# Performance work log

Hardware: AMD Instinct MI355X
Metric: run time of the kernel (lower is better)

The kernel has to match this reference:

```python
import jax, jax.numpy as jnp
import numpy as np

ALPHA = 0.5
B = 4096
K = 8192


def setup_inputs() -> dict:
    key = jax.random.key(0)
    k1, k2 = jax.random.split(key)
    outputs = jax.random.normal(k1, (B, K), dtype=jnp.float32)
    labels = jax.random.randint(k2, (B,), 0, K)
    targets = jax.nn.one_hot(labels, K, dtype=jnp.float32)
    S = jnp.eye(K, dtype=jnp.float32)          # soft-label matrix (state)
    S_t = jnp.zeros((K, K), dtype=jnp.float32)  # running stats (state)
    count = jnp.zeros((K, 1), dtype=jnp.float32)
    return {"outputs": outputs, "targets": targets, "S": S, "S_t": S_t, "count": count}


def reference(outputs, targets, S, S_t, count):
    # loss path
    ls = jax.nn.log_softmax(outputs, axis=1)          # [B, K]
    bsz = outputs.shape[0]
    target_label = jnp.argmax(targets, axis=1)        # [B]
    prediction = jnp.argmax(outputs, axis=1)          # [B]
    soft_targets = S[target_label]                    # [B, K] gather
    ce_hard = -(ls * targets).sum() / bsz
    ce_soft = -(ls * soft_targets).sum() / bsz
    loss = ALPHA * ce_hard + (1.0 - ALPHA) * ce_soft

    # stats accumulation (the original python for-loop, as one fused scatter-add)
    probs = jax.nn.softmax(jax.lax.stop_gradient(outputs), axis=1)  # [B, K]
    correct = (prediction == target_label).astype(probs.dtype)      # [B]
    S_t_new = S_t + jax.ops.segment_sum(probs * correct[:, None], target_label, num_segments=K)
    count_new = count + jax.ops.segment_sum(correct, target_label, num_segments=K)[:, None]
    return loss, S_t_new, count_new
```

## Files before the change

### kernel.cpp

```cpp
#include <hip/hip_runtime.h>
#include <math.h>

#define K 8192
#define BROWS 4096
#define ALPHA 0.5f

__device__ __forceinline__ void argmax_combine(float& v, int& i, float v2, int i2){
  if (v2 > v || (v2 == v && i2 < i)) { v = v2; i = i2; }
}

__global__ __launch_bounds__(256) void row_stats_kernel(
    const float* __restrict__ outputs,
    const float* __restrict__ targets,
    const float* __restrict__ S,
    float* __restrict__ rowloss,
    int*   __restrict__ rowtl,
    int*   __restrict__ rowcorrect,
    float* __restrict__ rowm,
    float* __restrict__ rowinvZ)
{
  const int b = blockIdx.x;
  const int t = threadIdx.x;
  const int lane = t & 63;
  const int wid  = t >> 6;

  const float4* orow = (const float4*)(outputs + (size_t)b * K);
  float x[32];
#pragma unroll
  for (int i = 0; i < 8; ++i){
    float4 v = orow[i*256 + t];
    x[4*i+0]=v.x; x[4*i+1]=v.y; x[4*i+2]=v.z; x[4*i+3]=v.w;
  }

  float mv = -INFINITY; int mi = 0x7fffffff;
#pragma unroll
  for (int i = 0; i < 8; ++i){
#pragma unroll
    for (int c = 0; c < 4; ++c){
      int idx = i*1024 + t*4 + c;
      argmax_combine(mv, mi, x[4*i+c], idx);
    }
  }

  const float4* trow = (const float4*)(targets + (size_t)b * K);
  float tv = -INFINITY; int ti = 0x7fffffff;
  float d_hard = 0.f, s_hard = 0.f;
#pragma unroll
  for (int i = 0; i < 8; ++i){
    float4 v = trow[i*256 + t];
    float tc[4] = {v.x, v.y, v.z, v.w};
#pragma unroll
    for (int c = 0; c < 4; ++c){
      int idx = i*1024 + t*4 + c;
      d_hard += x[4*i+c] * tc[c];
      s_hard += tc[c];
      argmax_combine(tv, ti, tc[c], idx);
    }
  }

#pragma unroll
  for (int off = 32; off; off >>= 1){
    float v2 = __shfl_down(mv, off, 64); int i2 = __shfl_down(mi, off, 64);
    argmax_combine(mv, mi, v2, i2);
    v2 = __shfl_down(tv, off, 64); i2 = __shfl_down(ti, off, 64);
    argmax_combine(tv, ti, v2, i2);
  }

  __shared__ float s_v[2][4]; __shared__ int s_i[2][4];
  __shared__ float s_m; __shared__ int s_pred; __shared__ int s_tl;
  if (lane == 0){ s_v[0][wid]=mv; s_i[0][wid]=mi; s_v[1][wid]=tv; s_i[1][wid]=ti; }
  __syncthreads();
  if (t == 0){
    float av=s_v[0][0]; int ai=s_i[0][0];
    float bv=s_v[1][0]; int bi=s_i[1][0];
#pragma unroll
    for (int w=1; w<4; ++w){
      argmax_combine(av, ai, s_v[0][w], s_i[0][w]);
      argmax_combine(bv, bi, s_v[1][w], s_i[1][w]);
    }
    s_m = av; s_pred = ai; s_tl = bi;
  }
  __syncthreads();
  const float m  = s_m;
  const int   tl = s_tl;

  float se = 0.f;
#pragma unroll
  for (int i = 0; i < 32; ++i) se += expf(x[i] - m);

  const float4* srow = (const float4*)(S + (size_t)tl * K);
  float d_soft = 0.f, s_soft = 0.f;
#pragma unroll
  for (int i = 0; i < 8; ++i){
    float4 v = srow[i*256 + t];
    d_soft += x[4*i+0]*v.x + x[4*i+1]*v.y + x[4*i+2]*v.z + x[4*i+3]*v.w;
    s_soft += v.x + v.y + v.z + v.w;
  }

  float sums[5] = {d_hard, s_hard, se, d_soft, s_soft};
#pragma unroll
  for (int off = 32; off; off >>= 1){
#pragma unroll
    for (int j = 0; j < 5; ++j) sums[j] += __shfl_down(sums[j], off, 64);
  }
  __shared__ float s_sums[4][5];
  if (lane == 0){
#pragma unroll
    for (int j = 0; j < 5; ++j) s_sums[wid][j] = sums[j];
  }
  __syncthreads();
  if (t == 0){
    float tot[5];
#pragma unroll
    for (int j=0;j<5;++j) tot[j] = s_sums[0][j]+s_sums[1][j]+s_sums[2][j]+s_sums[3][j];
    float Z = tot[2];
    float logZ = logf(Z);
    float ceh = -(tot[0] - (m + logZ) * tot[1]);
    float ces = -(tot[3] - (m + logZ) * tot[4]);
    rowloss[b]    = (ALPHA * ceh + (1.0f - ALPHA) * ces) * (1.0f / (float)BROWS);
    rowtl[b]      = tl;
    rowcorrect[b] = (s_pred == tl) ? 1 : 0;
    rowm[b]       = m;
    rowinvZ[b]    = 1.0f / Z;
  }
}

__global__ __launch_bounds__(256) void copy_st_kernel(const float* __restrict__ src,
                                                      float* __restrict__ dst){
  size_t base = (size_t)blockIdx.x * 8192 + threadIdx.x;
#pragma unroll
  for (int j = 0; j < 32; ++j)
    dst[base + (size_t)j*256] = src[base + (size_t)j*256];
}

__global__ __launch_bounds__(256) void loss_count_kernel(const float* __restrict__ rowloss,
                                                         const float* __restrict__ count,
                                                         float* __restrict__ out_loss,
                                                         float* __restrict__ out_count){
  int t = threadIdx.x;
  float s = 0.f;
  for (int i = t; i < BROWS; i += 256) s += rowloss[i];
#pragma unroll
  for (int off = 32; off; off >>= 1) s += __shfl_down(s, off, 64);
  __shared__ float sh[4];
  if ((t & 63) == 0) sh[t >> 6] = s;
  __syncthreads();
  if (t == 0) out_loss[0] = sh[0] + sh[1] + sh[2] + sh[3];
  for (int i = t; i < K; i += 256) out_count[i] = count[i];
}

__global__ __launch_bounds__(256) void scatter_kernel(const float* __restrict__ outputs,
    const int* __restrict__ rowtl, const int* __restrict__ rowcorrect,
    const float* __restrict__ rowm, const float* __restrict__ rowinvZ,
    float* __restrict__ out_St, float* __restrict__ out_count){
  int b = blockIdx.x;
  if (!rowcorrect[b]) return;
  int tl = rowtl[b];
  float m = rowm[b], invZ = rowinvZ[b];
  const float* orow = outputs + (size_t)b * K;
  float* drow = out_St + (size_t)tl * K;
  for (int k = threadIdx.x; k < K; k += 256)
    atomicAdd(&drow[k], expf(orow[k] - m) * invZ);
  if (threadIdx.x == 0) atomicAdd(&out_count[tl], 1.0f);
}

extern "C" void kernel_launch(void* const* d_in, const int* in_sizes, int n_in,
                              void* d_out, int out_size, void* d_ws, size_t ws_size,
                              hipStream_t stream) {
  const float* outputs = (const float*)d_in[0];
  const float* targets = (const float*)d_in[1];
  const float* S       = (const float*)d_in[2];
  const float* S_t     = (const float*)d_in[3];
  const float* count   = (const float*)d_in[4];

  float* out       = (float*)d_out;
  float* out_loss  = out;
  float* out_St    = out + 1;
  float* out_count = out + 1 + (size_t)K * K;

  float* rowloss    = (float*)d_ws;
  float* rowm       = rowloss + BROWS;
  float* rowinvZ    = rowm + BROWS;
  int*   rowtl      = (int*)(rowinvZ + BROWS);
  int*   rowcorrect = rowtl + BROWS;

  hipLaunchKernelGGL(row_stats_kernel, dim3(BROWS), dim3(256), 0, stream,
                     outputs, targets, S, rowloss, rowtl, rowcorrect, rowm, rowinvZ);
  hipLaunchKernelGGL(copy_st_kernel, dim3(8192), dim3(256), 0, stream, S_t, out_St);
  hipLaunchKernelGGL(loss_count_kernel, dim3(1), dim3(256), 0, stream,
                     rowloss, count, out_loss, out_count);
  hipLaunchKernelGGL(scatter_kernel, dim3(BROWS), dim3(256), 0, stream,
                     outputs, rowtl, rowcorrect, rowm, rowinvZ, out_St, out_count);
}
```

Baseline: 727.6 us.

## Fuse row stats with S_t copy and merge loss reduction into scatter kernel

Interleaves row-statistics blocks with S_t copy blocks in a single launch so the compute-heavy row pass overlaps the bandwidth-bound 256MB copy. The copy writes aligned float4 stores to the output (offset by one float for the loss slot) while reading scalars, and the count copy rides along in one copy block. The loss reduction and count copy kernel is folded into an extra block of the scatter kernel, cutting the launch count from four to two. Reads of S_t become unaligned scalar loads, which could reduce read efficiency.

```diff
diff --git a/kernel.cpp b/kernel.cpp
--- a/kernel.cpp
+++ b/kernel.cpp
@@ -4,27 +4,71 @@
 #define K 8192
 #define BROWS 4096
 #define ALPHA 0.5f
+#define NTOT ((size_t)K * (size_t)K)
+#define VEC4 16777215
 
 __device__ __forceinline__ void argmax_combine(float& v, int& i, float v2, int i2){
   if (v2 > v || (v2 == v && i2 < i)) { v = v2; i = i2; }
 }
 
-__global__ __launch_bounds__(256) void row_stats_kernel(
+__global__ __launch_bounds__(256) void fused_kernel(
     const float* __restrict__ outputs,
     const float* __restrict__ targets,
     const float* __restrict__ S,
+    const float* __restrict__ S_t,
+    const float* __restrict__ count,
+    float* __restrict__ out,
     float* __restrict__ rowloss,
     int*   __restrict__ rowtl,
     int*   __restrict__ rowcorrect,
     float* __restrict__ rowm,
     float* __restrict__ rowinvZ)
 {
-  const int b = blockIdx.x;
-  const int t = threadIdx.x;
+  __shared__ float s_v[2][4]; __shared__ int s_i[2][4];
+  __shared__ float s_m; __shared__ int s_pred; __shared__ int s_tl;
+  __shared__ float s_sums[4][5];
+
+  const int bb = blockIdx.x;
+  const int r  = bb / 3;
+  const int m3 = bb - r * 3;
+  const int t  = threadIdx.x;
   const int lane = t & 63;
   const int wid  = t >> 6;
 
-  const float4* orow = (const float4*)(outputs + (size_t)b * K);
+  if (m3 != 0) {
+    const int cb = 2 * r + (m3 - 1);
+    float4* dst4 = (float4*)(out + 4);
+    const size_t base = (size_t)cb * 2048 + t;
+    if (cb != 8191) {
+#pragma unroll
+      for (int i = 0; i < 8; ++i) {
+        size_t d = base + (size_t)i * 256;
+        size_t e = 4 * d + 3;
+        float4 v; v.x = S_t[e]; v.y = S_t[e+1]; v.z = S_t[e+2]; v.w = S_t[e+3];
+        dst4[d] = v;
+      }
+    } else {
+#pragma unroll
+      for (int i = 0; i < 8; ++i) {
+        size_t d = base + (size_t)i * 256;
+        if (d < (size_t)VEC4) {
+          size_t e = 4 * d + 3;
+          float4 v; v.x = S_t[e]; v.y = S_t[e+1]; v.z = S_t[e+2]; v.w = S_t[e+3];
+          dst4[d] = v;
+        }
+      }
+    }
+    if (cb == 0) {
+      if (t < 3) out[1 + t] = S_t[t];
+      if (t == 3) out[NTOT] = S_t[NTOT - 1];
+    } else if (cb == 1) {
+      float* out_count = out + 1 + NTOT;
+      for (int i = t; i < K; i += 256) out_count[i] = count[i];
+    }
+    return;
+  }
+
+  const float4* orow = (const float4*)(outputs + (size_t)r * K);
   float x[32];
 #pragma unroll
   for (int i = 0; i < 8; ++i){
@@ -42,7 +86,7 @@
     }
   }
 
-  const float4* trow = (const float4*)(targets + (size_t)b * K);
+  const float4* trow = (const float4*)(targets + (size_t)r * K);
   float tv = -INFINITY; int ti = 0x7fffffff;
   float d_hard = 0.f, s_hard = 0.f;
 #pragma unroll
@@ -66,8 +110,6 @@
     argmax_combine(tv, ti, v2, i2);
   }
 
-  __shared__ float s_v[2][4]; __shared__ int s_i[2][4];
-  __shared__ float s_m; __shared__ int s_pred; __shared__ int s_tl;
   if (lane == 0){ s_v[0][wid]=mv; s_i[0][wid]=mi; s_v[1][wid]=tv; s_i[1][wid]=ti; }
   __syncthreads();
   if (t == 0){
@@ -103,7 +145,6 @@
 #pragma unroll
     for (int j = 0; j < 5; ++j) sums[j] += __shfl_down(sums[j], off, 64);
   }
-  __shared__ float s_sums[4][5];
   if (lane == 0){
 #pragma unroll
     for (int j = 0; j < 5; ++j) s_sums[wid][j] = sums[j];
@@ -117,51 +158,44 @@
     float logZ = logf(Z);
     float ceh = -(tot[0] - (m + logZ) * tot[1]);
     float ces = -(tot[3] - (m + logZ) * tot[4]);
-    rowloss[b]    = (ALPHA * ceh + (1.0f - ALPHA) * ces) * (1.0f / (float)BROWS);
-    rowtl[b]      = tl;
-    rowcorrect[b] = (s_pred == tl) ? 1 : 0;
-    rowm[b]       = m;
-    rowinvZ[b]    = 1.0f / Z;
-  }
-}
-
-__global__ __launch_bounds__(256) void copy_st_kernel(const float* __restrict__ src,
-                                                      float* __restrict__ dst){
-  size_t base = (size_t)blockIdx.x * 8192 + threadIdx.x;
-#pragma unroll
-  for (int j = 0; j < 32; ++j)
-    dst[base + (size_t)j*256] = src[base + (size_t)j*256];
-}
-
-__global__ __launch_bounds__(256) void loss_count_kernel(const float* __restrict__ rowloss,
-                                                         const float* __restrict__ count,
-                                                         float* __restrict__ out_loss,
-                                                         float* __restrict__ out_count){
-  int t = threadIdx.x;
-  float s = 0.f;
-  for (int i = t; i < BROWS; i += 256) s += rowloss[i];
-#pragma unroll
-  for (int off = 32; off; off >>= 1) s += __shfl_down(s, off, 64);
-  __shared__ float sh[4];
-  if ((t & 63) == 0) sh[t >> 6] = s;
-  __syncthreads();
-  if (t == 0) out_loss[0] = sh[0] + sh[1] + sh[2] + sh[3];
-  for (int i = t; i < K; i += 256) out_count[i] = count[i];
-}
-
-__global__ __launch_bounds__(256) void scatter_kernel(const float* __restrict__ outputs,
-    const int* __restrict__ rowtl, const int* __restrict__ rowcorrect,
-    const float* __restrict__ rowm, const float* __restrict__ rowinvZ,
-    float* __restrict__ out_St, float* __restrict__ out_count){
-  int b = blockIdx.x;
+    rowloss[r]    = (ALPHA * ceh + (1.0f - ALPHA) * ces) * (1.0f / (float)BROWS);
+    rowtl[r]      = tl;
+    rowcorrect[r] = (s_pred == tl) ? 1 : 0;
+    rowm[r]       = m;
+    rowinvZ[r]    = 1.0f / Z;
+  }
+}
+
+__global__ __launch_bounds__(256) void epilogue_kernel(
+    const float* __restrict__ outputs,
+    const float* __restrict__ rowloss,
+    const int*   __restrict__ rowtl,
+    const int*   __restrict__ rowcorrect,
+    const float* __restrict__ rowm,
+    const float* __restrict__ rowinvZ,
+    float* __restrict__ out)
+{
+  const int b = blockIdx.x;
+  const int t = threadIdx.x;
+  if (b == BROWS) {
+    float s = 0.f;
+    for (int i = t; i < BROWS; i += 256) s += rowloss[i];
+#pragma unroll
+    for (int off = 32; off; off >>= 1) s += __shfl_down(s, off, 64);
+    __shared__ float sh[4];
+    if ((t & 63) == 0) sh[t >> 6] = s;
+    __syncthreads();
+    if (t == 0) out[0] = sh[0] + sh[1] + sh[2] + sh[3];
+    return;
+  }
   if (!rowcorrect[b]) return;
-  int tl = rowtl[b];
-  float m = rowm[b], invZ = rowinvZ[b];
+  const int tl = rowtl[b];
+  const float m = rowm[b], invZ = rowinvZ[b];
   const float* orow = outputs + (size_t)b * K;
-  float* drow = out_St + (size_t)tl * K;
-  for (int k = threadIdx.x; k < K; k += 256)
+  float* drow = out + 1 + (size_t)tl * K;
+  for (int k = t; k < K; k += 256)
     atomicAdd(&drow[k], expf(orow[k] - m) * invZ);
-  if (threadIdx.x == 0) atomicAdd(&out_count[tl], 1.0f);
+  if (t == 0) atomicAdd(out + 1 + NTOT + tl, 1.0f);
 }
 
 extern "C" void kernel_launch(void* const* d_in, const int* in_sizes, int n_in,
@@ -173,10 +207,7 @@
   const float* S_t     = (const float*)d_in[3];
   const float* count   = (const float*)d_in[4];
 
-  float* out       = (float*)d_out;
-  float* out_loss  = out;
-  float* out_St    = out + 1;
-  float* out_count = out + 1 + (size_t)K * K;
+  float* out = (float*)d_out;
 
   float* rowloss    = (float*)d_ws;
   float* rowm       = rowloss + BROWS;
@@ -184,11 +215,9 @@
   int*   rowtl      = (int*)(rowinvZ + BROWS);
   int*   rowcorrect = rowtl + BROWS;
 
-  hipLaunchKernelGGL(row_stats_kernel, dim3(BROWS), dim3(256), 0, stream,
-                     outputs, targets, S, rowloss, rowtl, rowcorrect, rowm, rowinvZ);
-  hipLaunchKernelGGL(copy_st_kernel, dim3(8192), dim3(256), 0, stream, S_t, out_St);
-  hipLaunchKernelGGL(loss_count_kernel, dim3(1), dim3(256), 0, stream,
-                     rowloss, count, out_loss, out_count);
-  hipLaunchKernelGGL(scatter_kernel, dim3(BROWS), dim3(256), 0, stream,
-                     outputs, rowtl, rowcorrect, rowm, rowinvZ, out_St, out_count);
-}
+  hipLaunchKernelGGL(fused_kernel, dim3(3 * BROWS), dim3(256), 0, stream,
+                     outputs, targets, S, S_t, count, out,
+                     rowloss, rowtl, rowcorrect, rowm, rowinvZ);
+  hipLaunchKernelGGL(epilogue_kernel, dim3(BROWS + 1), dim3(256), 0, stream,
+                     outputs, rowloss, rowtl, rowcorrect, rowm, rowinvZ, out);
+}
```

Result: no change. 723.7 us (-0.5%).
